# Performance work log

Measured on AMD Instinct MI355X. Metric: run time of the kernel, lower is better.

## Reference

```python
import jax, jax.numpy as jnp
import numpy as np

B, L, D, H, VOCAB = 8, 1024, 1024, 8, 32000
DH = D // H  # dim_per_head = 128
SCALE = float((DH // H) ** (-0.5))  # faithful to key.size(-1)//num_heads
EPS = 1e-5


def setup_inputs() -> dict:
    key = jax.random.key(0)
    ks = jax.random.split(key, 12)
    tokens = jax.random.randint(ks[0], (B, L), 0, VOCAB)
    s = 0.02
    emb = jax.random.normal(ks[1], (VOCAB, D), jnp.float32) * s
    emb = emb.at[0].set(0.0)  # padding_idx=0
    Wq = jax.random.normal(ks[2], (D, D), jnp.float32) * s
    Wk = jax.random.normal(ks[3], (D, D), jnp.float32) * s
    Wv = jax.random.normal(ks[4], (D, D), jnp.float32) * s
    Wo = jax.random.normal(ks[5], (D, D), jnp.float32) * s
    bq = jnp.zeros((D,), jnp.float32)
    bk = jnp.zeros((D,), jnp.float32)
    bv = jnp.zeros((D,), jnp.float32)
    bo = jnp.zeros((D,), jnp.float32)
    gamma = jnp.ones((2 * D,), jnp.float32)
    beta = jnp.zeros((2 * D,), jnp.float32)
    return {"tokens": tokens, "emb": emb, "Wq": Wq, "bq": bq, "Wk": Wk,
            "bk": bk, "Wv": Wv, "bv": bv, "Wo": Wo, "bo": bo,
            "gamma": gamma, "beta": beta}


def reference(tokens, emb, Wq, bq, Wk, bk, Wv, bv, Wo, bo, gamma, beta):
    # padding mask: [B, L, L] True where key token == 0
    pad = (tokens == 0)  # [B, L]
    mask = jnp.broadcast_to(pad[:, None, :], (B, L, L))
    mask = jnp.tile(mask, (H, 1, 1))  # torch .repeat(num_heads,1,1) -> [H*B, L, L]

    x = emb[tokens]  # [B, L, D]

    q = (x @ Wq + bq).reshape(B * H, L, DH)  # faithful interleaved view
    k = (x @ Wk + bk).reshape(B * H, L, DH)
    v = (x @ Wv + bv).reshape(B * H, L, DH)

    scores = jnp.einsum('bqd,bkd->bqk', q, k) * SCALE
    scores = jnp.where(mask, -jnp.inf, scores)
    attn = jax.nn.softmax(scores, axis=-1)
    ctx = jnp.einsum('bqk,bkd->bqd', attn, v).reshape(B, L, D)

    out = ctx @ Wo + bo  # [B, L, D]
    r = x + out
    maxpool = r.max(axis=1)   # [B, D]
    meanpool = r.mean(axis=1)  # [B, D]
    agg = jnp.concatenate([maxpool, meanpool], axis=1)  # [B, 2D]

    mu = agg.mean(axis=-1, keepdims=True)
    var = agg.var(axis=-1, keepdims=True)
    return (agg - mu) / jnp.sqrt(var + EPS) * gamma + beta
```

## Files before the change

kernel.cpp:

```cpp
#include <hip/hip_runtime.h>
#include <math.h>

typedef __attribute__((ext_vector_type(8))) short short8;
typedef __attribute__((ext_vector_type(4))) float f32x4;

constexpr int CB = 8, CL = 1024, CD = 1024, CDH = 128, CM = 8192;
constexpr float CSCALE = 0.25f;
constexpr float CEPS = 1e-5f;

__device__ inline ushort f2b(float f) {
    union { float f; unsigned u; } v; v.f = f;
    unsigned r = v.u + 0x7FFF + ((v.u >> 16) & 1);
    return (ushort)(r >> 16);
}
__device__ inline float b2f(ushort u) {
    union { unsigned u; float f; } v; v.u = ((unsigned)u) << 16;
    return v.f;
}

__device__ inline void gld16(const void* g, void* l) {
    __builtin_amdgcn_global_load_lds(
        (const __attribute__((address_space(1))) void*)g,
        (__attribute__((address_space(3))) void*)l, 16, 0, 0);
}

__global__ __launch_bounds__(256) void k_gather(const int* __restrict__ tokens,
                                                const float* __restrict__ emb,
                                                float* __restrict__ x,
                                                ushort* __restrict__ xb) {
    int row = blockIdx.x;
    int tok = tokens[row];
    float4 v = ((const float4*)(emb + (size_t)tok * CD))[threadIdx.x];
    ((float4*)(x + (size_t)row * CD))[threadIdx.x] = v;
    ushort4 o; o.x = f2b(v.x); o.y = f2b(v.y); o.z = f2b(v.z); o.w = f2b(v.w);
    ((ushort4*)(xb + (size_t)row * CD))[threadIdx.x] = o;
}

__global__ __launch_bounds__(256) void k_wtrans(const float* __restrict__ W,
                                                ushort* __restrict__ Wt) {
    __shared__ float ws_[32][33];
    const int tk = blockIdx.x * 32, tn = blockIdx.y * 32;
    const int t = threadIdx.x;
    {
        int r = t >> 3, c4 = (t & 7) * 4;
        *(float4*)&ws_[r][c4] = *(const float4*)&W[(size_t)(tk + r) * CD + tn + c4];
    }
    __syncthreads();
    int n = t >> 3, k4 = (t & 7) * 4;
    ushort4 o;
    o.x = f2b(ws_[k4 + 0][n]); o.y = f2b(ws_[k4 + 1][n]);
    o.z = f2b(ws_[k4 + 2][n]); o.w = f2b(ws_[k4 + 3][n]);
    *(ushort4*)&Wt[(size_t)(tn + n) * CD + tk + k4] = o;
}

__device__ inline void stage24(const ushort* __restrict__ A,
                               const ushort* __restrict__ B,
                               ushort* ldsA, ushort* ldsB,
                               int bm, int bn, int kbase,
                               int w, int lane15, int quad, int l) {
    #pragma unroll
    for (int c = 0; c < 3; ++c) {
        int pid = w * 3 + c;
        if (pid < 16)
            gld16(A + (size_t)(bm + pid * 16 + lane15) * CD + kbase + quad * 8,
                  ldsA + pid * 512 + (size_t)l * 8);
        else
            gld16(B + (size_t)(bn + (pid - 16) * 16 + lane15) * CD + kbase + quad * 8,
                  ldsB + (pid - 16) * 512 + (size_t)l * 8);
    }
}

#define GEMM_PIPELINE(Aptr, Bptr)                                                  \
    f32x4 acc[4][4] = {};                                                          \
    stage24(Aptr, Bptr, &As_[0][0][0][0], &Bs_[0][0][0][0], bm, bn, 0,             \
            w, lane15, quad, l);                                                   \
    stage24(Aptr, Bptr, &As_[0][1][0][0], &Bs_[0][1][0][0], bm, bn, 32,            \
            w, lane15, quad, l);                                                   \
    asm volatile("s_waitcnt vmcnt(3)" ::: "memory");                               \
    __builtin_amdgcn_s_barrier();                                                  \
    int cur = 0;                                                                   \
    for (int kt = 0; kt < 16; ++kt) {                                              \
        const int nk = (kt + 1) & 15;                                              \
        _Pragma("unroll")                                                          \
        for (int kh = 0; kh < 2; ++kh) {                                           \
            short8 af[4], bf[4];                                                   \
            _Pragma("unroll")                                                      \
            for (int im = 0; im < 4; ++im)                                         \
                af[im] = *(const short8*)&As_[cur][kh][wr * 4 + im][(size_t)l * 8];\
            _Pragma("unroll")                                                      \
            for (int in = 0; in < 4; ++in)                                         \
                bf[in] = *(const short8*)&Bs_[cur][kh][wc * 4 + in][(size_t)l * 8];\
            stage24(Aptr, Bptr, &As_[cur ^ 1][kh][0][0], &Bs_[cur ^ 1][kh][0][0],  \
                    bm, bn, nk * 64 + kh * 32, w, lane15, quad, l);                \
            __builtin_amdgcn_s_barrier();                                          \
            asm volatile("s_waitcnt lgkmcnt(0)" ::: "memory");                     \
            __builtin_amdgcn_s_setprio(1);                                         \
            _Pragma("unroll")                                                      \
            for (int im = 0; im < 4; ++im)                                         \
                _Pragma("unroll")                                                  \
                for (int in = 0; in < 4; ++in)                                     \
                    acc[im][in] = __builtin_amdgcn_mfma_f32_16x16x32_bf16(         \
                        af[im], bf[in], acc[im][in], 0, 0, 0);                     \
            __builtin_amdgcn_s_setprio(0);                                         \
            asm volatile("s_waitcnt vmcnt(3)" ::: "memory");                       \
            __builtin_amdgcn_s_barrier();                                          \
        }                                                                          \
        cur ^= 1;                                                                  \
    }                                                                              \
    asm volatile("s_waitcnt vmcnt(0)" ::: "memory");

__global__ __launch_bounds__(512, 2) void k_gemm_qkv(const ushort* __restrict__ A,
                                                     const ushort* __restrict__ Wt3,
                                                     const float* __restrict__ b0,
                                                     const float* __restrict__ b1,
                                                     const float* __restrict__ b2,
                                                     ushort* __restrict__ C3) {
    __shared__ ushort As_[2][2][16][512];
    __shared__ ushort Bs_[2][2][8][512];
    const int t = threadIdx.x, w = t >> 6, l = t & 63;
    const int lane15 = l & 15, quad = l >> 4;
    const int wr = w >> 1, wc = w & 1;
    const int bx = blockIdx.x, by = blockIdx.y;
    const int bm = by * 256, bn = bx * 128;

    GEMM_PIPELINE(A, Wt3)

    const int z = bx >> 3;
    const float* bias = (z == 0) ? b0 : ((z == 1) ? b1 : b2);
    ushort* Cout = C3 + (size_t)z * CM * CD;
    const int colbase = (bx & 7) * 128 + wc * 64;
    #pragma unroll
    for (int in = 0; in < 4; ++in) {
        int col = colbase + in * 16 + lane15;
        float bv = bias[col];
        #pragma unroll
        for (int im = 0; im < 4; ++im) {
            int row0 = bm + wr * 64 + im * 16 + quad * 4;
            #pragma unroll
            for (int r = 0; r < 4; ++r)
                Cout[(size_t)(row0 + r) * CD + col] = f2b(acc[im][in][r] + bv);
        }
    }
}

__global__ __launch_bounds__(512, 2) void k_gemm_out(const ushort* __restrict__ A,
                                                     const ushort* __restrict__ Bt,
                                                     const float* __restrict__ bias,
                                                     const float* __restrict__ resid,
                                                     float* __restrict__ pmax,
                                                     float* __restrict__ psum) {
    __shared__ ushort As_[2][2][16][512];
    __shared__ ushort Bs_[2][2][8][512];
    __shared__ float redmx[8][64], redsm[8][64];
    const int t = threadIdx.x, w = t >> 6, l = t & 63;
    const int lane15 = l & 15, quad = l >> 4;
    const int wr = w >> 1, wc = w & 1;
    const int bx = blockIdx.x, by = blockIdx.y;
    const int bm = by * 256, bn = bx * 128;

    GEMM_PIPELINE(A, Bt)

    const int bb = by >> 2, chunk = by & 3;
    float vmax_[4], vsum_[4];
    #pragma unroll
    for (int in = 0; in < 4; ++in) {
        int col = bn + wc * 64 + in * 16 + lane15;
        float bvv = bias[col];
        float mx = -3.4e38f, sm = 0.f;
        #pragma unroll
        for (int im = 0; im < 4; ++im) {
            int row0 = bm + wr * 64 + im * 16 + quad * 4;
            #pragma unroll
            for (int r = 0; r < 4; ++r) {
                float rel = acc[im][in][r] + bvv + resid[(size_t)(row0 + r) * CD + col];
                mx = fmaxf(mx, rel);
                sm += rel;
            }
        }
        mx = fmaxf(mx, __shfl_xor(mx, 16));
        mx = fmaxf(mx, __shfl_xor(mx, 32));
        sm += __shfl_xor(sm, 16);
        sm += __shfl_xor(sm, 32);
        vmax_[in] = mx; vsum_[in] = sm;
    }
    if (l < 16) {
        #pragma unroll
        for (int in = 0; in < 4; ++in) {
            redmx[w][in * 16 + lane15] = vmax_[in];
            redsm[w][in * 16 + lane15] = vsum_[in];
        }
    }
    __syncthreads();
    if (t < 128) {
        int wc2 = t >> 6, cc = t & 63;
        float m = redmx[wc2][cc], s = redsm[wc2][cc];
        #pragma unroll
        for (int j = 1; j < 4; ++j) {
            m = fmaxf(m, redmx[j * 2 + wc2][cc]);
            s += redsm[j * 2 + wc2][cc];
        }
        size_t off = ((size_t)bb * 4 + chunk) * CD + bn + wc2 * 64 + cc;
        pmax[off] = m;
        psum[off] = s;
    }
}

__global__ __launch_bounds__(256) void k_vtransp(const ushort* __restrict__ v,
                                                 ushort* __restrict__ Vtp) {
    __shared__ ushort Vs[64 * 136];
    const int i = blockIdx.x >> 4, kt = blockIdx.x & 15;
    const ushort* src = v + (size_t)i * 131072 + (size_t)kt * 64 * 128;
    const int t = threadIdx.x;
    #pragma unroll
    for (int ii = 0; ii < 4; ++ii) {
        int idx = t + 256 * ii;
        int key = idx >> 4, seg = idx & 15;
        *(uint4*)&Vs[key * 136 + seg * 8] = *(const uint4*)&src[key * 128 + seg * 8];
    }
    __syncthreads();
    ushort* dst = Vtp + (size_t)blockIdx.x * 8192;
    #pragma unroll
    for (int it = 0; it < 4; ++it) {
        int L = t + 256 * it;
        int cell = L & 63;
        int quadk = cell >> 4, l15 = cell & 15;
        int p = L >> 6;
        int d = (p >> 1) * 16 + l15;
        int kb = ((p & 1) * 4 + quadk) * 8;
        uint pk[4];
        #pragma unroll
        for (int jj = 0; jj < 4; ++jj) {
            uint lo = Vs[(kb + 2 * jj) * 136 + d];
            uint hi = Vs[(kb + 2 * jj + 1) * 136 + d];
            pk[jj] = lo | (hi << 16);
        }
        *(uint4*)&dst[(size_t)L * 8] = *(uint4*)pk;
    }
}

__global__ __launch_bounds__(512) void k_attn(const ushort* __restrict__ Q,
                                              const ushort* __restrict__ K,
                                              const ushort* __restrict__ Vtp,
                                              const int* __restrict__ tokens,
                                              ushort* __restrict__ ctx) {
    __shared__ ushort Ks[16 * 512];
    __shared__ ushort Vs[16 * 512];
    __shared__ ushort Ps[8 * 1088];
    __shared__ ushort Msk[CL];
    const int i = blockIdx.x, qb = blockIdx.y * 128;
    const int t = threadIdx.x, w = t >> 6, l = t & 63;
    const int lane15 = l & 15, quad = l >> 4;

    {
        const int* tokb = tokens + (i & 7) * CL;
        #pragma unroll
        for (int jj = 0; jj < 2; ++jj) {
            int idx = t + 512 * jj;
            Msk[idx] = (tokb[idx] == 0) ? (ushort)0xFF80 : (ushort)0;
        }
    }
    const int qrow = qb + w * 16 + lane15;
    short8 af[4];
    #pragma unroll
    for (int kc = 0; kc < 4; ++kc)
        af[kc] = *(const short8*)&Q[(size_t)i * 131072 + (size_t)qrow * 128 + kc * 32 + quad * 8];

    f32x4 oacc[8];
    #pragma unroll
    for (int dt = 0; dt < 8; ++dt) oacc[dt] = f32x4{0.f, 0.f, 0.f, 0.f};
    float lsum[4] = {0.f, 0.f, 0.f, 0.f};
    const int wbase = w * 1088;

    for (int kt = 0; kt < 16; ++kt) {
        __syncthreads();
        #pragma unroll
        for (int c = 0; c < 2; ++c) {
            int p = w * 2 + c;
            gld16(K + (size_t)i * 131072 + (size_t)(kt * 64 + (p >> 2) * 16 + lane15) * 128
                    + (p & 3) * 32 + quad * 8,
                  &Ks[p * 512 + l * 8]);
            gld16(Vtp + ((size_t)(i * 16 + kt) * 16 + p) * 512 + l * 8,
                  &Vs[p * 512 + l * 8]);
        }
        __syncthreads();

        f32x4 sc[4];
        #pragma unroll
        for (int j = 0; j < 4; ++j) {
            sc[j] = f32x4{0.f, 0.f, 0.f, 0.f};
            #pragma unroll
            for (int kc = 0; kc < 4; ++kc) {
                short8 bk = *(const short8*)&Ks[(j * 4 + kc) * 512 + l * 8];
                sc[j] = __builtin_amdgcn_mfma_f32_16x16x32_bf16(af[kc], bk, sc[j], 0, 0, 0);
            }
        }
        #pragma unroll
        for (int j = 0; j < 4; ++j) {
            float mj = b2f(Msk[kt * 64 + j * 16 + lane15]);
            #pragma unroll
            for (int r = 0; r < 4; ++r) {
                float p = __expf(fmaf(sc[j][r], CSCALE, mj));
                sc[j][r] = p;
                lsum[r] += p;
            }
        }
        #pragma unroll
        for (int j = 0; j < 4; ++j) {
            int ks2 = j >> 1;
            int qq  = (j & 1) * 2 + (lane15 >> 3);
            int pos = lane15 & 7;
            #pragma unroll
            for (int r = 0; r < 4; ++r) {
                union { float f; unsigned u; } cv; cv.f = sc[j][r];
                Ps[wbase + ks2 * 544 + qq * 136 + (quad * 4 + r) * 8 + pos] =
                    (ushort)(cv.u >> 16);
            }
        }
        short8 ap[2];
        #pragma unroll
        for (int ks2 = 0; ks2 < 2; ++ks2)
            ap[ks2] = *(const short8*)&Ps[wbase + ks2 * 544 + quad * 136 + lane15 * 8];
        #pragma unroll
        for (int dt = 0; dt < 8; ++dt)
            #pragma unroll
            for (int ks2 = 0; ks2 < 2; ++ks2) {
                short8 bv = *(const short8*)&Vs[(dt * 2 + ks2) * 512 + l * 8];
                oacc[dt] = __builtin_amdgcn_mfma_f32_16x16x32_bf16(ap[ks2], bv, oacc[dt], 0, 0, 0);
            }
    }
    float inv[4];
    #pragma unroll
    for (int r = 0; r < 4; ++r) {
        float s = lsum[r];
        #pragma unroll
        for (int off = 1; off < 16; off <<= 1) s += __shfl_xor(s, off);
        inv[r] = 1.f / s;
    }
    #pragma unroll
    for (int dt = 0; dt < 8; ++dt)
        #pragma unroll
        for (int r = 0; r < 4; ++r) {
            int q = qb + w * 16 + quad * 4 + r;
            ctx[(size_t)i * 131072 + (size_t)q * 128 + dt * 16 + lane15] =
                f2b(oacc[dt][r] * inv[r]);
        }
}

__global__ __launch_bounds__(1024) void k_pool2(const float* __restrict__ pmax,
                                                const float* __restrict__ psum,
                                                const float* __restrict__ gamma,
                                                const float* __restrict__ beta,
                                                float* __restrict__ out) {
    __shared__ float rs[16], rq[16];
    __shared__ float s_mu, s_inv;
    const int b = blockIdx.x;
    const int d = threadIdx.x;
    float mx = -3.4e38f, sm = 0.f;
    #pragma unroll
    for (int c = 0; c < 4; ++c) {
        size_t off = ((size_t)b * 4 + c) * CD + d;
        mx = fmaxf(mx, pmax[off]);
        sm += psum[off];
    }
    const float a0 = mx;
    const float a1 = sm * (1.0f / 1024.0f);
    float s = a0 + a1;
    float qd = a0 * a0 + a1 * a1;
    #pragma unroll
    for (int off = 32; off > 0; off >>= 1) {
        s  += __shfl_xor(s, off);
        qd += __shfl_xor(qd, off);
    }
    const int wid = d >> 6;
    if ((d & 63) == 0) { rs[wid] = s; rq[wid] = qd; }
    __syncthreads();
    if (d == 0) {
        float S = 0.f, Qm = 0.f;
        for (int ww = 0; ww < 16; ++ww) { S += rs[ww]; Qm += rq[ww]; }
        float mu  = S * (1.0f / 2048.0f);
        float var = Qm * (1.0f / 2048.0f) - mu * mu;
        s_mu = mu; s_inv = 1.0f / sqrtf(var + CEPS);
    }
    __syncthreads();
    const float mu = s_mu, inv = s_inv;
    out[(size_t)b * 2048 + d]        = (a0 - mu) * inv * gamma[d]        + beta[d];
    out[(size_t)b * 2048 + 1024 + d] = (a1 - mu) * inv * gamma[1024 + d] + beta[1024 + d];
}

extern "C" void kernel_launch(void* const* d_in, const int* in_sizes, int n_in,
                              void* d_out, int out_size, void* d_ws, size_t ws_size,
                              hipStream_t stream) {
    const int*   tokens = (const int*)d_in[0];
    const float* emb    = (const float*)d_in[1];
    const float* Wq     = (const float*)d_in[2];
    const float* bq     = (const float*)d_in[3];
    const float* Wk     = (const float*)d_in[4];
    const float* bk     = (const float*)d_in[5];
    const float* Wv     = (const float*)d_in[6];
    const float* bv     = (const float*)d_in[7];
    const float* Wo     = (const float*)d_in[8];
    const float* bo     = (const float*)d_in[9];
    const float* gamma  = (const float*)d_in[10];
    const float* beta   = (const float*)d_in[11];
    float* out = (float*)d_out;

    char* p = (char*)d_ws;
    float*  x   = (float*)p;   p += (size_t)CM * CD * 4;
    ushort* xb  = (ushort*)p;  p += (size_t)CM * CD * 2;
    ushort* wqt = (ushort*)p;  p += (size_t)CD * CD * 2;
    ushort* wkt = (ushort*)p;  p += (size_t)CD * CD * 2;
    ushort* wvt = (ushort*)p;  p += (size_t)CD * CD * 2;
    ushort* wot = (ushort*)p;  p += (size_t)CD * CD * 2;
    ushort* qb_ = (ushort*)p;  p += (size_t)CM * CD * 2;
    ushort* kb_ = (ushort*)p;  p += (size_t)CM * CD * 2;
    ushort* vb_ = (ushort*)p;  p += (size_t)CM * CD * 2;
    ushort* Vtp = (ushort*)p;  p += (size_t)CM * CD * 2;
    float*  pmax = (float*)p;  p += (size_t)CB * 4 * CD * 4;
    float*  psum = (float*)p;  p += (size_t)CB * 4 * CD * 4;
    ushort* ctx = vb_;

    k_gather<<<CM, 256, 0, stream>>>(tokens, emb, x, xb);

    dim3 wg(32, 32);
    k_wtrans<<<wg, 256, 0, stream>>>(Wq, wqt);
    k_wtrans<<<wg, 256, 0, stream>>>(Wk, wkt);
    k_wtrans<<<wg, 256, 0, stream>>>(Wv, wvt);
    k_wtrans<<<wg, 256, 0, stream>>>(Wo, wot);

    dim3 gq(3 * CD / 128, CM / 256);
    k_gemm_qkv<<<gq, 512, 0, stream>>>(xb, wqt, bq, bk, bv, qb_);

    k_vtransp<<<64 * 16, 256, 0, stream>>>(vb_, Vtp);

    dim3 ag(64, 8);
    k_attn<<<ag, 512, 0, stream>>>(qb_, kb_, Vtp, tokens, ctx);

    dim3 go(CD / 128, CM / 256);
    k_gemm_out<<<go, 512, 0, stream>>>(ctx, wot, bo, x, pmax, psum);

    k_pool2<<<CB, 1024, 0, stream>>>(pmax, psum, gamma, beta, out);
}
```

Baseline: 379.5 us.

## Use six-stage LDS ring pipeline and XCD-aware block swizzle in GEMMs

Replaces the double-buffered GEMM main loop with a six-slot LDS ring that keeps five K-slices in flight and needs one barrier per step instead of two. Both GEMM launches become 1D grids whose block index is remapped so that blocks on the same XCD share row and column tiles, aiming for better L2 reuse. LDS use rises to about 144KB per block, which may cut occupancy below the two blocks per CU the launch bounds request. The tail prefetch loads a clamped slice again, which is redundant work.

Result: no change. 386.1 us (+1.7%).

```diff
diff --git a/kernel.cpp b/kernel.cpp
--- a/kernel.cpp
+++ b/kernel.cpp
@@ -70,44 +70,41 @@
     }
 }
 
-#define GEMM_PIPELINE(Aptr, Bptr)                                                  \
+#define GEMM_RING(Aptr, Bptr)                                                      \
     f32x4 acc[4][4] = {};                                                          \
-    stage24(Aptr, Bptr, &As_[0][0][0][0], &Bs_[0][0][0][0], bm, bn, 0,             \
-            w, lane15, quad, l);                                                   \
-    stage24(Aptr, Bptr, &As_[0][1][0][0], &Bs_[0][1][0][0], bm, bn, 32,            \
-            w, lane15, quad, l);                                                   \
-    asm volatile("s_waitcnt vmcnt(3)" ::: "memory");                               \
-    __builtin_amdgcn_s_barrier();                                                  \
-    int cur = 0;                                                                   \
-    for (int kt = 0; kt < 16; ++kt) {                                              \
-        const int nk = (kt + 1) & 15;                                              \
+    _Pragma("unroll")                                                              \
+    for (int q = 0; q < 5; ++q)                                                    \
+        stage24(Aptr, Bptr, &As_[q][0][0], &Bs_[q][0][0], bm, bn,                  \
+                (q >> 1) * 64 + (q & 1) * 32, w, lane15, quad, l);                 \
+    int rd = 0, st = 5;                                                            \
+    _Pragma("unroll 2")                                                            \
+    for (int p = 0; p < 32; ++p) {                                                 \
+        asm volatile("s_waitcnt vmcnt(12)" ::: "memory");                          \
+        __builtin_amdgcn_s_barrier();                                              \
+        short8 af[4], bf[4];                                                       \
         _Pragma("unroll")                                                          \
-        for (int kh = 0; kh < 2; ++kh) {                                           \
-            short8 af[4], bf[4];                                                   \
-            _Pragma("unroll")                                                      \
-            for (int im = 0; im < 4; ++im)                                         \
-                af[im] = *(const short8*)&As_[cur][kh][wr * 4 + im][(size_t)l * 8];\
+        for (int im = 0; im < 4; ++im)                                             \
+            af[im] = *(const short8*)&As_[rd][wr * 4 + im][(size_t)l * 8];         \
+        _Pragma("unroll")                                                          \
+        for (int in = 0; in < 4; ++in)                                             \
+            bf[in] = *(const short8*)&Bs_[rd][wc * 4 + in][(size_t)l * 8];         \
+        int kx = p + 5; if (kx > 31) kx = 31;                                      \
+        stage24(Aptr, Bptr, &As_[st][0][0], &Bs_[st][0][0], bm, bn,                \
+                (kx >> 1) * 64 + (kx & 1) * 32, w, lane15, quad, l);               \
+        asm volatile("s_waitcnt lgkmcnt(0)" ::: "memory");                         \
+        __builtin_amdgcn_s_setprio(1);                                             \
+        _Pragma("unroll")                                                          \
+        for (int im = 0; im < 4; ++im)                                             \
             _Pragma("unroll")                                                      \
             for (int in = 0; in < 4; ++in)                                         \
-                bf[in] = *(const short8*)&Bs_[cur][kh][wc * 4 + in][(size_t)l * 8];\
-            stage24(Aptr, Bptr, &As_[cur ^ 1][kh][0][0], &Bs_[cur ^ 1][kh][0][0],  \
-                    bm, bn, nk * 64 + kh * 32, w, lane15, quad, l);                \
-            __builtin_amdgcn_s_barrier();                                          \
-            asm volatile("s_waitcnt lgkmcnt(0)" ::: "memory");                     \
-            __builtin_amdgcn_s_setprio(1);                                         \
-            _Pragma("unroll")                                                      \
-            for (int im = 0; im < 4; ++im)                                         \
-                _Pragma("unroll")                                                  \
-                for (int in = 0; in < 4; ++in)                                     \
-                    acc[im][in] = __builtin_amdgcn_mfma_f32_16x16x32_bf16(         \
-                        af[im], bf[in], acc[im][in], 0, 0, 0);                     \
-            __builtin_amdgcn_s_setprio(0);                                         \
-            asm volatile("s_waitcnt vmcnt(3)" ::: "memory");                       \
-            __builtin_amdgcn_s_barrier();                                          \
-        }                                                                          \
-        cur ^= 1;                                                                  \
+                acc[im][in] = __builtin_amdgcn_mfma_f32_16x16x32_bf16(             \
+                    af[im], bf[in], acc[im][in], 0, 0, 0);                         \
+        __builtin_amdgcn_s_setprio(0);                                             \
+        rd = (rd == 5) ? 0 : rd + 1;                                               \
+        st = (st == 5) ? 0 : st + 1;                                               \
     }                                                                              \
-    asm volatile("s_waitcnt vmcnt(0)" ::: "memory");
+    asm volatile("s_waitcnt vmcnt(0)" ::: "memory");                               \
+    __builtin_amdgcn_s_barrier();
 
 __global__ __launch_bounds__(512, 2) void k_gemm_qkv(const ushort* __restrict__ A,
                                                      const ushort* __restrict__ Wt3,
@@ -115,15 +112,18 @@
                                                      const float* __restrict__ b1,
                                                      const float* __restrict__ b2,
                                                      ushort* __restrict__ C3) {
-    __shared__ ushort As_[2][2][16][512];
-    __shared__ ushort Bs_[2][2][8][512];
+    __shared__ ushort As_[6][16][512];
+    __shared__ ushort Bs_[6][8][512];
     const int t = threadIdx.x, w = t >> 6, l = t & 63;
     const int lane15 = l & 15, quad = l >> 4;
     const int wr = w >> 1, wc = w & 1;
-    const int bx = blockIdx.x, by = blockIdx.y;
+    const int id = blockIdx.x;
+    const int xcd = id & 7, off = id >> 3;
+    const int bx = (xcd & 1) * 12 + off % 12;
+    const int by = (xcd >> 1) * 8 + off / 12;
     const int bm = by * 256, bn = bx * 128;
 
-    GEMM_PIPELINE(A, Wt3)
+    GEMM_RING(A, Wt3)
 
     const int z = bx >> 3;
     const float* bias = (z == 0) ? b0 : ((z == 1) ? b1 : b2);
@@ -149,16 +149,19 @@
                                                      const float* __restrict__ resid,
                                                      float* __restrict__ pmax,
                                                      float* __restrict__ psum) {
-    __shared__ ushort As_[2][2][16][512];
-    __shared__ ushort Bs_[2][2][8][512];
+    __shared__ ushort As_[6][16][512];
+    __shared__ ushort Bs_[6][8][512];
     __shared__ float redmx[8][64], redsm[8][64];
     const int t = threadIdx.x, w = t >> 6, l = t & 63;
     const int lane15 = l & 15, quad = l >> 4;
     const int wr = w >> 1, wc = w & 1;
-    const int bx = blockIdx.x, by = blockIdx.y;
+    const int id = blockIdx.x;
+    const int xcd = id & 7, off = id >> 3;
+    const int bx = (xcd & 1) * 4 + (off & 3);
+    const int by = (xcd >> 1) * 8 + (off >> 2);
     const int bm = by * 256, bn = bx * 128;
 
-    GEMM_PIPELINE(A, Bt)
+    GEMM_RING(A, Bt)
 
     const int bb = by >> 2, chunk = by & 3;
     float vmax_[4], vsum_[4];
@@ -199,9 +202,9 @@
             m = fmaxf(m, redmx[j * 2 + wc2][cc]);
             s += redsm[j * 2 + wc2][cc];
         }
-        size_t off = ((size_t)bb * 4 + chunk) * CD + bn + wc2 * 64 + cc;
-        pmax[off] = m;
-        psum[off] = s;
+        size_t off2 = ((size_t)bb * 4 + chunk) * CD + bn + wc2 * 64 + cc;
+        pmax[off2] = m;
+        psum[off2] = s;
     }
 }
 
@@ -427,16 +430,14 @@
     k_wtrans<<<wg, 256, 0, stream>>>(Wv, wvt);
     k_wtrans<<<wg, 256, 0, stream>>>(Wo, wot);
 
-    dim3 gq(3 * CD / 128, CM / 256);
-    k_gemm_qkv<<<gq, 512, 0, stream>>>(xb, wqt, bq, bk, bv, qb_);
+    k_gemm_qkv<<<768, 512, 0, stream>>>(xb, wqt, bq, bk, bv, qb_);
 
     k_vtransp<<<64 * 16, 256, 0, stream>>>(vb_, Vtp);
 
     dim3 ag(64, 8);
     k_attn<<<ag, 512, 0, stream>>>(qb_, kb_, Vtp, tokens, ctx);
 
-    dim3 go(CD / 128, CM / 256);
-    k_gemm_out<<<go, 512, 0, stream>>>(ctx, wot, bo, x, pmax, psum);
+    k_gemm_out<<<256, 512, 0, stream>>>(ctx, wot, bo, x, pmax, psum);
 
     k_pool2<<<CB, 1024, 0, stream>>>(pmax, psum, gamma, beta, out);
 }
```
